# Kernel tuning notes

Hardware: AMD Instinct MI355X
Metric: run time of the kernel (lower is better)

## Reference

```python
import jax, jax.numpy as jnp
import numpy as np

DIM = 3072      # model dim (Qwen-Image)
HEADS = 24
HD = 128        # head dim; inner = HEADS*HD = 3072
INNER = HEADS * HD
FF = 4 * DIM    # 12288
S_IMG = 1024
S_TXT = 256
S_TOT = S_IMG + S_TXT
B = 1
EPS = 1e-6
SCALE_SHIFT = 1.0


def setup_inputs() -> dict:
    key = jax.random.key(0)
    ks = iter(jax.random.split(key, 64))
    W = 0.02

    def nrm(shape, s=W):
        return jax.random.normal(next(ks), shape, dtype=jnp.float32) * s

    # RoPE tables for the joint (txt first, then img) sequence, interleaved layout
    pos = jnp.arange(S_TOT, dtype=jnp.float32)
    inv = 1.0 / (10000.0 ** (jnp.arange(HD // 2, dtype=jnp.float32) / (HD // 2)))
    ang = pos[:, None] * inv[None, :]                       # [S, HD/2]
    rope_cos = jnp.repeat(jnp.cos(ang), 2, axis=-1)         # [S, HD]
    rope_sin = jnp.repeat(jnp.sin(ang), 2, axis=-1)

    inp = {
        "hidden_states": jax.random.normal(next(ks), (B, S_IMG, DIM), dtype=jnp.float32),
        "encoder_hidden_states": jax.random.normal(next(ks), (B, S_TXT, DIM), dtype=jnp.float32),
        "temb": jax.random.normal(next(ks), (B, DIM), dtype=jnp.float32),
        "rope_cos": rope_cos,
        "rope_sin": rope_sin,
        # modulation (AWQW4A16Linear equivalent)
        "img_mod_w": nrm((6 * DIM, DIM)), "img_mod_b": nrm((6 * DIM,)),
        "txt_mod_w": nrm((6 * DIM, DIM)), "txt_mod_b": nrm((6 * DIM,)),
        # attention (SVDQW4A4Linear equivalents)
        "qkv_w": nrm((3 * INNER, DIM)), "qkv_b": nrm((3 * INNER,)),
        "add_qkv_w": nrm((3 * INNER, DIM)), "add_qkv_b": nrm((3 * INNER,)),
        "norm_q_g": jnp.ones((HD,), jnp.float32), "norm_k_g": jnp.ones((HD,), jnp.float32),
        "norm_added_q_g": jnp.ones((HD,), jnp.float32), "norm_added_k_g": jnp.ones((HD,), jnp.float32),
        "to_out_w": nrm((DIM, INNER)), "to_out_b": nrm((DIM,)),
        "to_add_out_w": nrm((DIM, INNER)), "to_add_out_b": nrm((DIM,)),
        # MLPs
        "img_mlp_w1": nrm((FF, DIM)), "img_mlp_b1": nrm((FF,)),
        "img_mlp_w2": nrm((DIM, FF)), "img_mlp_b2": nrm((DIM,)),
        "txt_mlp_w1": nrm((FF, DIM)), "txt_mlp_b1": nrm((FF,)),
        "txt_mlp_w2": nrm((DIM, FF)), "txt_mlp_b2": nrm((DIM,)),
    }
    return inp


def _lin(x, w, b):
    return jnp.matmul(x, w.T) + b


def _ln(x):  # LayerNorm, no affine, eps=1e-6
    mu = jnp.mean(x, axis=-1, keepdims=True)
    var = jnp.mean(jnp.square(x - mu), axis=-1, keepdims=True)
    return (x - mu) * jax.lax.rsqrt(var + EPS)


def _rms(x, g):  # per-head RMSNorm over last dim (HD)
    ms = jnp.mean(jnp.square(x), axis=-1, keepdims=True)
    return x * jax.lax.rsqrt(ms + EPS) * g


def _rope(x, cos, sin):  # x: [B,S,H,D], cos/sin: [S,D], interleaved rotate
    x1 = x[..., 0::2]
    x2 = x[..., 1::2]
    xr = jnp.stack([-x2, x1], axis=-1).reshape(x.shape)
    return x * cos[None, :, None, :] + xr * sin[None, :, None, :]


def _reorder_mod(m):
    # view(B,-1,6).transpose(1,2).reshape(B,-1): de-interleave 6 modulation vecs
    b = m.shape[0]
    return m.reshape(b, DIM, 6).transpose(0, 2, 1).reshape(b, 6 * DIM)


def _modulate(x, mod):
    shift, scale, gate = jnp.split(mod, 3, axis=-1)
    return x * (scale + SCALE_SHIFT)[:, None, :] + shift[:, None, :], gate[:, None, :]


def _mlp(x, w1, b1, w2, b2):  # GELU(tanh) MLP
    h = jax.nn.gelu(_lin(x, w1, b1), approximate=True)
    return _lin(h, w2, b2)


def reference(hidden_states, encoder_hidden_states, temb, rope_cos, rope_sin,
              img_mod_w, img_mod_b, txt_mod_w, txt_mod_b,
              qkv_w, qkv_b, add_qkv_w, add_qkv_b,
              norm_q_g, norm_k_g, norm_added_q_g, norm_added_k_g,
              to_out_w, to_out_b, to_add_out_w, to_add_out_b,
              img_mlp_w1, img_mlp_b1, img_mlp_w2, img_mlp_b2,
              txt_mlp_w1, txt_mlp_b1, txt_mlp_w2, txt_mlp_b2):
    b = hidden_states.shape[0]

    img_mod = _reorder_mod(_lin(jax.nn.silu(temb), img_mod_w, img_mod_b))
    txt_mod = _reorder_mod(_lin(jax.nn.silu(temb), txt_mod_w, txt_mod_b))
    img_mod1, img_mod2 = jnp.split(img_mod, 2, axis=-1)
    txt_mod1, txt_mod2 = jnp.split(txt_mod, 2, axis=-1)

    img_modulated, img_gate1 = _modulate(_ln(hidden_states), img_mod1)
    txt_modulated, txt_gate1 = _modulate(_ln(encoder_hidden_states), txt_mod1)

    # ---- joint attention ----
    img_q, img_k, img_v = jnp.split(_lin(img_modulated, qkv_w, qkv_b), 3, axis=-1)
    txt_q, txt_k, txt_v = jnp.split(_lin(txt_modulated, add_qkv_w, add_qkv_b), 3, axis=-1)

    def heads(x):  # [B,S,INNER] -> [B,S,H,HD]
        return x.reshape(b, x.shape[1], HEADS, HD)

    img_q = _rms(heads(img_q), norm_q_g)
    img_k = _rms(heads(img_k), norm_k_g)
    txt_q = _rms(heads(txt_q), norm_added_q_g)
    txt_k = _rms(heads(txt_k), norm_added_k_g)

    q = jnp.concatenate([txt_q, img_q], axis=1)  # txt first
    k = jnp.concatenate([txt_k, img_k], axis=1)
    v = jnp.concatenate([heads(txt_v), heads(img_v)], axis=1)

    q = _rope(q, rope_cos, rope_sin)
    k = _rope(k, rope_cos, rope_sin)

    scale = 1.0 / jnp.sqrt(jnp.float32(HD))
    scores = jnp.einsum('bqhd,bkhd->bhqk', q, k) * scale
    probs = jax.nn.softmax(scores, axis=-1)
    attn = jnp.einsum('bhqk,bkhd->bqhd', probs, v).reshape(b, S_TOT, INNER)

    txt_attn = attn[:, :S_TXT, :]
    img_attn = attn[:, S_TXT:, :]
    img_attn = _lin(img_attn, to_out_w, to_out_b)
    txt_attn = _lin(txt_attn, to_add_out_w, to_add_out_b)

    hidden_states = hidden_states + img_gate1 * img_attn
    encoder_hidden_states = encoder_hidden_states + txt_gate1 * txt_attn

    # ---- MLPs ----
    img_m2, img_gate2 = _modulate(_ln(hidden_states), img_mod2)
    hidden_states = hidden_states + img_gate2 * _mlp(img_m2, img_mlp_w1, img_mlp_b1, img_mlp_w2, img_mlp_b2)

    txt_m2, txt_gate2 = _modulate(_ln(encoder_hidden_states), txt_mod2)
    encoder_hidden_states = encoder_hidden_states + txt_gate2 * _mlp(txt_m2, txt_mlp_w1, txt_mlp_b1, txt_mlp_w2, txt_mlp_b2)

    return (encoder_hidden_states, hidden_states)
```

## Files before the change

kernel.cpp:

```cpp
#include <hip/hip_runtime.h>

#define DIMC   3072
#define HEADS  24
#define HD     128
#define FF     12288
#define S_IMG  1024
#define S_TXT  256
#define S_TOT  1280
#define EPSF   1e-6f

typedef __attribute__((ext_vector_type(8))) short bf16x8;
typedef __attribute__((ext_vector_type(4))) float f32x4;
typedef __attribute__((ext_vector_type(4))) float float4v;
typedef __attribute__((ext_vector_type(4))) unsigned int u32x4;
typedef __attribute__((ext_vector_type(2))) unsigned int u32x2;

__device__ __forceinline__ unsigned short f2bf(float f) {
    union { float f; unsigned u; } c; c.f = f;
    unsigned u = c.u;
    unsigned r = (u + 0x7fffu + ((u >> 16) & 1u)) >> 16;
    return (unsigned short)r;
}
__device__ __forceinline__ float b2f(unsigned short h) {
    union { unsigned u; float f; } c; c.u = ((unsigned)h) << 16;
    return c.f;
}
__device__ __forceinline__ unsigned packbf(float a, float b) {
    union { float f; unsigned u; } x, y; x.f = a; y.f = b;
    return __builtin_amdgcn_perm(y.u + 0x8000u, x.u + 0x8000u, 0x07060302);
}
__device__ __forceinline__ float gelu_tanh(float v) {
    float u = 1.5957691216057308f * (v + 0.044715f * v * v * v);
    float e = __expf(u);
    float t = 1.0f - 2.0f / (e + 1.0f);
    return 0.5f * v * (1.0f + t);
}

#define GLL16(gsrc, ldst)                                                     \
    __builtin_amdgcn_global_load_lds(                                         \
        (const __attribute__((address_space(1))) void*)(gsrc),                \
        (__attribute__((address_space(3))) void*)(ldst), 16, 0, 0)

struct SwpArgs {
    const float* W;
    const unsigned short* X;
    const float* bias;
    unsigned short* out;
};

template<int EPI>
__global__ __launch_bounds__(512, 2)
void gemm_swp(SwpArgs g0, SwpArgs g1, int nxW, int padx, int K, int ldout)
{
    int bx, sTile;
    SwpArgs g;
    {
        const int id = blockIdx.x;
        const int imgN = padx * 4;
        if (id < imgN) {
            int xcd = id & 7, t = id >> 3;
            int j = t & 3, slot = t >> 2;
            bx = slot * 8 + xcd;
            if (bx >= nxW) return;
            g = g0; sTile = j * 256;
        } else {
            bx = id - imgN;
            g = g1; sTile = 0;
        }
    }
    const int bm = bx * 256;

    __shared__ __align__(16) char smem[131072];
    char* smemW = smem;
    char* smemX = smem + 65536;

    const int tid  = threadIdx.x;
    const int lane = tid & 63;
    const int wave = tid >> 6;
    const int wm = wave >> 2, wc = wave & 3;

    const int pW  = tid & 7;
    const int rW0 = tid >> 3;
    const int swW = (rW0 & 7) << 4;
    const int rX = lane >> 3;
    const int cX = (lane & 7) ^ rX;

    float4v wreg[4][2];

    auto WLOAD = [&](int t) {
        const float* src = g.W + (long)t * 64 + pW * 8;
        #pragma unroll
        for (int i = 0; i < 4; i++) {
            const float* p = src + (long)(bm + rW0 + i * 64) * K;
            wreg[i][0] = *(const float4v*)p;
            wreg[i][1] = *(const float4v*)(p + 4);
        }
    };
    auto WSTORE = [&](int buf) {
        #pragma unroll
        for (int i = 0; i < 4; i++) {
            int r = rW0 + i * 64;
            u32x4 w;
            w[0] = packbf(wreg[i][0][0], wreg[i][0][1]);
            w[1] = packbf(wreg[i][0][2], wreg[i][0][3]);
            w[2] = packbf(wreg[i][1][0], wreg[i][1][1]);
            w[3] = packbf(wreg[i][1][2], wreg[i][1][3]);
            *(u32x4*)(smemW + buf * 32768 + r * 128 + ((pW * 16) ^ swW)) = w;
        }
    };
    auto XSTAGE = [&](int buf, int t) {
        const long kof = (long)t * 64 + cX * 8;
        #pragma unroll
        for (int i = 0; i < 4; i++) {
            int r = i * 64 + wave * 8 + rX;
            GLL16(g.X + (long)(sTile + r) * K + kof,
                  smemX + buf * 32768 + i * 8192 + wave * 1024);
        }
    };

    f32x4 acc[8][4] = {};
    auto COMPUTE = [&](int buf) {
        #pragma unroll
        for (int ks = 0; ks < 2; ks++) {
            const int kb = ks * 64 + (lane >> 4) * 16;
            bf16x8 wf[8], xf[4];
            #pragma unroll
            for (int mi = 0; mi < 8; mi++) {
                int r = wm * 128 + mi * 16 + (lane & 15);
                wf[mi] = *(const bf16x8*)(smemW + buf * 32768 + r * 128 + (kb ^ ((r & 7) << 4)));
            }
            #pragma unroll
            for (int ni = 0; ni < 4; ni++) {
                int r = wc * 64 + ni * 16 + (lane & 15);
                xf[ni] = *(const bf16x8*)(smemX + buf * 32768 + r * 128 + (kb ^ ((r & 7) << 4)));
            }
            #pragma unroll
            for (int mi = 0; mi < 8; mi++)
                #pragma unroll
                for (int ni = 0; ni < 4; ni++)
                    acc[mi][ni] = __builtin_amdgcn_mfma_f32_16x16x32_bf16(
                        wf[mi], xf[ni], acc[mi][ni], 0, 0, 0);
        }
    };

    const int nk = K >> 6;
    WLOAD(0);
    XSTAGE(0, 0);
    WSTORE(0);
    __syncthreads();
    for (int t = 0; t < nk; ++t) {
        const int cur = t & 1;
        if (t + 1 < nk) {
            WLOAD(t + 1);
            XSTAGE(cur ^ 1, t + 1);
        }
        __builtin_amdgcn_sched_barrier(0);
        COMPUTE(cur);
        __builtin_amdgcn_sched_barrier(0);
        if (t + 1 < nk) WSTORE(cur ^ 1);
        __syncthreads();
    }

    #pragma unroll
    for (int mi = 0; mi < 8; mi++) {
        int m0 = wm * 128 + mi * 16 + ((lane >> 4) << 2);
        float4v bv = *(const float4v*)(g.bias + bm + m0);
        #pragma unroll
        for (int ni = 0; ni < 4; ni++) {
            int n = wc * 64 + ni * 16 + (lane & 15);
            float v0 = acc[mi][ni][0] + bv[0];
            float v1 = acc[mi][ni][1] + bv[1];
            float v2 = acc[mi][ni][2] + bv[2];
            float v3 = acc[mi][ni][3] + bv[3];
            if constexpr (EPI == 2) {
                v0 = gelu_tanh(v0); v1 = gelu_tanh(v1);
                v2 = gelu_tanh(v2); v3 = gelu_tanh(v3);
            }
            u32x2 w;
            w[0] = packbf(v0, v1);
            w[1] = packbf(v2, v3);
            *(u32x2*)(smem + n * 512 + ((2 * m0) ^ ((n & 31) << 4))) = w;
        }
    }
    __syncthreads();
    {
        const int s = tid >> 1;
        const int cbase = (tid & 1) * 16;
        unsigned short* orow = g.out + (long)(sTile + s) * ldout + bm;
        #pragma unroll
        for (int c = 0; c < 16; c++) {
            int chunk = cbase + c;
            u32x4 d = *(const u32x4*)(smem + s * 512 + ((chunk * 16) ^ ((s & 31) << 4)));
            *(u32x4*)(orow + chunk * 8) = d;
        }
    }
}

struct GemmArgs {
    const unsigned short* A;
    const void* B;
    const float* bias;
    void* out;
    long bOut;
};

template<int EPI, bool BF16B, bool SWZ>
__global__ __launch_bounds__(256)
void gemm_bt(GemmArgs g0, GemmArgs g1, int ysplit,
             int K, int lda, int ldb, int ldout,
             long batchA, long batchB, int nbn, int nby)
{
    int by, bnIdx, z;
    if constexpr (SWZ) {
        const int id = blockIdx.x;
        const int xcd = id & 7, t = id >> 3;
        const int j = t % 10;
        const int slot = t / 10;
        const int gidx = slot * 8 + xcd;
        by = j; bnIdx = gidx % nbn; z = gidx / nbn;
        (void)nby;
    } else {
        by = blockIdx.y; bnIdx = blockIdx.x; z = blockIdx.z;
    }

    __shared__ __align__(16) char smem[65536];
    char* smemA = smem;
    char* smemB = smem + 32768;

    const int tid  = threadIdx.x;
    const int lane = tid & 63;
    const int wave = tid >> 6;
    const int wm = wave >> 1, wc = wave & 1;

    const bool second = (by >= ysplit);
    const GemmArgs g = second ? g1 : g0;
    const int bm = (second ? by - ysplit : by) * 128;
    const int bn = bnIdx * 128;

    const unsigned short* A = g.A + (long)z * batchA;
    const float* Bf = (const float*)g.B + (long)z * batchB;
    const unsigned short* Bh = (const unsigned short*)g.B + (long)z * batchB;

    const int rA = lane >> 3;
    const int cA = (lane & 7) ^ rA;
    const int pB = tid & 7;
    const int rB0 = tid >> 3;
    const int swB = (rB0 & 7) << 4;

    float4v breg[4][2];

    auto BLOAD = [&](int t) {
        const float* src = Bf + (long)t * 64 + pB * 8;
        #pragma unroll
        for (int i = 0; i < 4; i++) {
            const float* p = src + (long)(bn + rB0 + i * 32) * ldb;
            breg[i][0] = *(const float4v*)p;
            breg[i][1] = *(const float4v*)(p + 4);
        }
    };
    auto STAGE_A = [&](int buf, int t) {
        const long kof = (long)t * 64 + cA * 8;
        #pragma unroll
        for (int i = 0; i < 4; i++) {
            int r = i * 32 + wave * 8 + rA;
            GLL16(A + (long)(bm + r) * lda + kof,
                  smemA + buf * 16384 + i * 4096 + wave * 1024);
        }
    };
    auto STAGE_B16 = [&](int buf, int t) {
        const long kof = (long)t * 64 + cA * 8;
        #pragma unroll
        for (int i = 0; i < 4; i++) {
            int r = i * 32 + wave * 8 + rA;
            GLL16(Bh + (long)(bn + r) * ldb + kof,
                  smemB + buf * 16384 + i * 4096 + wave * 1024);
        }
    };
    auto BSTORE = [&](int buf) {
        #pragma unroll
        for (int i = 0; i < 4; i++) {
            int r = rB0 + i * 32;
            u32x4 w;
            w[0] = packbf(breg[i][0][0], breg[i][0][1]);
            w[1] = packbf(breg[i][0][2], breg[i][0][3]);
            w[2] = packbf(breg[i][1][0], breg[i][1][1]);
            w[3] = packbf(breg[i][1][2], breg[i][1][3]);
            *(u32x4*)(smemB + buf * 16384 + r * 128 + ((pB * 16) ^ swB)) = w;
        }
    };

    f32x4 acc[4][4] = {};
    auto COMPUTE = [&](int buf) {
        #pragma unroll
        for (int ks = 0; ks < 2; ks++) {
            const int kb = ks * 64 + (lane >> 4) * 16;
            bf16x8 af[4], bfr[4];
            #pragma unroll
            for (int mi = 0; mi < 4; mi++) {
                int r = wm * 64 + mi * 16 + (lane & 15);
                af[mi] = *(const bf16x8*)(smemA + buf * 16384 + r * 128 + (kb ^ ((r & 7) << 4)));
            }
            #pragma unroll
            for (int ni = 0; ni < 4; ni++) {
                int r = wc * 64 + ni * 16 + (lane & 15);
                bfr[ni] = *(const bf16x8*)(smemB + buf * 16384 + r * 128 + (kb ^ ((r & 7) << 4)));
            }
            #pragma unroll
            for (int mi = 0; mi < 4; mi++)
                #pragma unroll
                for (int ni = 0; ni < 4; ni++)
                    acc[mi][ni] = __builtin_amdgcn_mfma_f32_16x16x32_bf16(
                        af[mi], bfr[ni], acc[mi][ni], 0, 0, 0);
        }
    };

    const int nk = K >> 6;
    if constexpr (BF16B) {
        STAGE_A(0, 0); STAGE_B16(0, 0);
    } else {
        BLOAD(0); STAGE_A(0, 0); BSTORE(0);
    }
    __syncthreads();
    for (int t = 0; t < nk; ++t) {
        const int cur = t & 1;
        if (t + 1 < nk) {
            if constexpr (BF16B) {
                STAGE_A(cur ^ 1, t + 1); STAGE_B16(cur ^ 1, t + 1);
            } else {
                BLOAD(t + 1); STAGE_A(cur ^ 1, t + 1);
            }
        }
        __builtin_amdgcn_sched_barrier(0);
        COMPUTE(cur);
        __builtin_amdgcn_sched_barrier(0);
        if constexpr (!BF16B) { if (t + 1 < nk) BSTORE(cur ^ 1); }
        __syncthreads();
    }

    unsigned short* outh = (unsigned short*)g.out + (long)z * g.bOut;
    float*          outf = (float*)g.out + (long)z * g.bOut;
    #pragma unroll
    for (int mi = 0; mi < 4; mi++) {
        #pragma unroll
        for (int ni = 0; ni < 4; ni++) {
            int n = bn + wc * 64 + ni * 16 + (lane & 15);
            float bv = g.bias ? g.bias[n] : 0.0f;
            #pragma unroll
            for (int r = 0; r < 4; r++) {
                int m = bm + wm * 64 + mi * 16 + (lane >> 4) * 4 + r;
                float v = acc[mi][ni][r] + bv;
                long o = (long)m * ldout + n;
                if constexpr (EPI == 0)      outf[o] = v;
                else                         outh[o] = f2bf(v);
            }
        }
    }
}

__global__ void silu_k(const float* __restrict__ x, float* __restrict__ out) {
    int i = blockIdx.x * 256 + threadIdx.x;
    if (i < DIMC) { float v = x[i]; out[i] = v / (1.0f + expf(-v)); }
}

__global__ __launch_bounds__(256)
void mod_gemv(const float* __restrict__ st,
              const float* __restrict__ Wimg, const float* __restrict__ bimg,
              const float* __restrict__ Wtxt, const float* __restrict__ btxt,
              float* __restrict__ mimg, float* __restrict__ mtxt)
{
    int wv = threadIdx.x >> 6, lane = threadIdx.x & 63;
    int r = blockIdx.x * 4 + wv;
    const float* W = blockIdx.y ? Wtxt : Wimg;
    const float* b = blockIdx.y ? btxt : bimg;
    float* out = blockIdx.y ? mtxt : mimg;
    const float* row = W + (long)r * DIMC;
    float acc = 0.f;
    #pragma unroll
    for (int j = 0; j < 12; j++) {
        float4v wvv = ((const float4v*)row)[lane + j * 64];
        float4v xv  = ((const float4v*)st)[lane + j * 64];
        acc += wvv[0] * xv[0] + wvv[1] * xv[1] + wvv[2] * xv[2] + wvv[3] * xv[3];
    }
    #pragma unroll
    for (int o = 32; o; o >>= 1) acc += __shfl_xor(acc, o);
    if (lane == 0) {
        int d = r / 6, j6 = r % 6;
        out[j6 * DIMC + d] = acc + b[r];
    }
}

__global__ __launch_bounds__(256)
void ln_mod(const float* __restrict__ x, const float* __restrict__ shift,
            const float* __restrict__ scale, unsigned short* __restrict__ out)
{
    __shared__ float red[8];
    long row = blockIdx.x;
    const float* xr = x + row * DIMC;
    float4v v[3];
    float sum = 0.f, sq = 0.f;
    #pragma unroll
    for (int j = 0; j < 3; j++) {
        v[j] = ((const float4v*)xr)[threadIdx.x + j * 256];
        #pragma unroll
        for (int c = 0; c < 4; c++) { sum += v[j][c]; sq += v[j][c] * v[j][c]; }
    }
    int lane = threadIdx.x & 63, wv = threadIdx.x >> 6;
    #pragma unroll
    for (int o = 32; o; o >>= 1) { sum += __shfl_xor(sum, o); sq += __shfl_xor(sq, o); }
    if (lane == 0) { red[wv] = sum; red[4 + wv] = sq; }
    __syncthreads();
    sum = red[0] + red[1] + red[2] + red[3];
    sq  = red[4] + red[5] + red[6] + red[7];
    float mu = sum / DIMC;
    float var = sq / DIMC - mu * mu;
    float rstd = rsqrtf(var + EPSF);
    #pragma unroll
    for (int j = 0; j < 3; j++) {
        int nb = (threadIdx.x + j * 256) * 4;
        #pragma unroll
        for (int c = 0; c < 4; c++) {
            int n = nb + c;
            float y = (v[j][c] - mu) * rstd * (scale[n] + 1.0f) + shift[n];
            out[row * DIMC + n] = f2bf(y);
        }
    }
}

__global__ __launch_bounds__(256)
void reduce_ln(const float* __restrict__ p0, const float* __restrict__ p1,
               const float* __restrict__ pbias, const float* __restrict__ base,
               const float* __restrict__ gate1, const float* __restrict__ shift2,
               const float* __restrict__ scale2,
               float* __restrict__ h1, unsigned short* __restrict__ mA)
{
    __shared__ float red[8];
    long off = (long)blockIdx.x * DIMC;
    float4v v[3];
    float sum = 0.f, sq = 0.f;
    #pragma unroll
    for (int j = 0; j < 3; j++) {
        int idx = threadIdx.x + j * 256;
        float4v a  = ((const float4v*)(base + off))[idx];
        float4v q0 = ((const float4v*)(p0 + off))[idx];
        float4v q1 = ((const float4v*)(p1 + off))[idx];
        float4v gb = ((const float4v*)pbias)[idx];
        float4v gt = ((const float4v*)gate1)[idx];
        #pragma unroll
        for (int c = 0; c < 4; c++) {
            float val = a[c] + gt[c] * (gb[c] + q0[c] + q1[c]);
            v[j][c] = val; sum += val; sq += val * val;
        }
        ((float4v*)(h1 + off))[idx] = v[j];
    }
    int lane = threadIdx.x & 63, wv = threadIdx.x >> 6;
    #pragma unroll
    for (int o = 32; o; o >>= 1) { sum += __shfl_xor(sum, o); sq += __shfl_xor(sq, o); }
    if (lane == 0) { red[wv] = sum; red[4 + wv] = sq; }
    __syncthreads();
    sum = red[0] + red[1] + red[2] + red[3];
    sq  = red[4] + red[5] + red[6] + red[7];
    float mu = sum / DIMC;
    float rstd = rsqrtf(sq / DIMC - mu * mu + EPSF);
    #pragma unroll
    for (int j = 0; j < 3; j++) {
        int nb = (threadIdx.x + j * 256) * 4;
        #pragma unroll
        for (int c = 0; c < 4; c++) {
            int n = nb + c;
            float y = (v[j][c] - mu) * rstd * (scale2[n] + 1.0f) + shift2[n];
            mA[off + n] = f2bf(y);
        }
    }
}

__global__ __launch_bounds__(256)
void reduce_out(const float* __restrict__ p, long PS,
                const float* __restrict__ h1, const float* __restrict__ wbias,
                const float* __restrict__ gate2, float* __restrict__ out, int n4)
{
    int i = blockIdx.x * 256 + threadIdx.x;
    if (i >= n4) return;
    int n = (i * 4) % DIMC;
    float4v s = ((const float4v*)p)[i];
    float4v s1 = ((const float4v*)(p + PS))[i];
    float4v s2 = ((const float4v*)(p + 2 * PS))[i];
    float4v s3 = ((const float4v*)(p + 3 * PS))[i];
    float4v h = ((const float4v*)h1)[i];
    float4v bv = *(const float4v*)(wbias + n);
    float4v gv = *(const float4v*)(gate2 + n);
    float4v r;
    #pragma unroll
    for (int c = 0; c < 4; c++)
        r[c] = h[c] + gv[c] * (bv[c] + s[c] + s1[c] + s2[c] + s3[c]);
    ((float4v*)out)[i] = r;
}

__global__ __launch_bounds__(256)
void qkv_post(const unsigned short* __restrict__ qkv_img,
              const unsigned short* __restrict__ qkv_txt,
              const float* __restrict__ nqg, const float* __restrict__ nkg,
              const float* __restrict__ naqg, const float* __restrict__ nakg,
              const float* __restrict__ rc, const float* __restrict__ rs,
              unsigned short* __restrict__ q, unsigned short* __restrict__ k,
              unsigned short* __restrict__ vt)
{
    int s = blockIdx.x;
    int h = blockIdx.y * 4 + (threadIdx.x >> 6);
    int d0 = threadIdx.x & 63;
    const unsigned short* src;
    const float *gq, *gk;
    if (s < S_TXT) { src = qkv_txt + (long)s * 3 * DIMC; gq = naqg; gk = nakg; }
    else           { src = qkv_img + (long)(s - S_TXT) * 3 * DIMC; gq = nqg; gk = nkg; }

    float q0 = b2f(src[h * HD + d0]),            q1 = b2f(src[h * HD + d0 + 64]);
    float k0 = b2f(src[DIMC + h * HD + d0]),     k1 = b2f(src[DIMC + h * HD + d0 + 64]);
    float v0 = b2f(src[2 * DIMC + h * HD + d0]), v1 = b2f(src[2 * DIMC + h * HD + d0 + 64]);

    float sqq = q0 * q0 + q1 * q1;
    float sqk = k0 * k0 + k1 * k1;
    #pragma unroll
    for (int o = 32; o; o >>= 1) { sqq += __shfl_xor(sqq, o); sqk += __shfl_xor(sqk, o); }
    float rq = rsqrtf(sqq / (float)HD + EPSF);
    float rk = rsqrtf(sqk / (float)HD + EPSF);
    q0 *= rq * gq[d0]; q1 *= rq * gq[d0 + 64];
    k0 *= rk * gk[d0]; k1 *= rk * gk[d0 + 64];

    float qp0 = __shfl_xor(q0, 1), qp1 = __shfl_xor(q1, 1);
    float kp0 = __shfl_xor(k0, 1), kp1 = __shfl_xor(k1, 1);
    float c0 = rc[(long)s * HD + d0], c1 = rc[(long)s * HD + d0 + 64];
    float s0 = rs[(long)s * HD + d0], s1 = rs[(long)s * HD + d0 + 64];
    float sgn = (d0 & 1) ? 1.0f : -1.0f;
    float qo0 = q0 * c0 + sgn * qp0 * s0;
    float qo1 = q1 * c1 + sgn * qp1 * s1;
    float ko0 = k0 * c0 + sgn * kp0 * s0;
    float ko1 = k1 * c1 + sgn * kp1 * s1;

    const float scl = 0.08838834764831845f;
    long qkbase = ((long)h * S_TOT + s) * HD;
    q[qkbase + d0]      = f2bf(qo0 * scl);
    q[qkbase + d0 + 64] = f2bf(qo1 * scl);
    k[qkbase + d0]      = f2bf(ko0);
    k[qkbase + d0 + 64] = f2bf(ko1);
    vt[((long)h * HD + d0) * S_TOT + s]        = f2bf(v0);
    vt[((long)h * HD + d0 + 64) * S_TOT + s]   = f2bf(v1);
}

__global__ __launch_bounds__(256)
void softmax_k(unsigned short* __restrict__ scores)
{
    long row = (long)blockIdx.x * 4 + (threadIdx.x >> 6);
    int lane = threadIdx.x & 63;
    unsigned short* p = scores + row * S_TOT;
    float v[20];
    float mx = -1e30f;
    #pragma unroll
    for (int j = 0; j < 20; j++) { v[j] = b2f(p[lane + j * 64]); mx = fmaxf(mx, v[j]); }
    #pragma unroll
    for (int o = 32; o; o >>= 1) mx = fmaxf(mx, __shfl_xor(mx, o));
    float sum = 0.f;
    #pragma unroll
    for (int j = 0; j < 20; j++) { v[j] = __expf(v[j] - mx); sum += v[j]; }
    #pragma unroll
    for (int o = 32; o; o >>= 1) sum += __shfl_xor(sum, o);
    float inv = 1.0f / sum;
    #pragma unroll
    for (int j = 0; j < 20; j++) p[lane + j * 64] = f2bf(v[j] * inv);
}

extern "C" void kernel_launch(void* const* d_in, const int* in_sizes, int n_in,
                              void* d_out, int out_size, void* d_ws, size_t ws_size,
                              hipStream_t stream)
{
    const float* hidden   = (const float*)d_in[0];
    const float* enc      = (const float*)d_in[1];
    const float* temb     = (const float*)d_in[2];
    const float* rope_cos = (const float*)d_in[3];
    const float* rope_sin = (const float*)d_in[4];
    const float* img_mod_w = (const float*)d_in[5];
    const float* img_mod_b = (const float*)d_in[6];
    const float* txt_mod_w = (const float*)d_in[7];
    const float* txt_mod_b = (const float*)d_in[8];
    const float* qkv_w     = (const float*)d_in[9];
    const float* qkv_b     = (const float*)d_in[10];
    const float* add_qkv_w = (const float*)d_in[11];
    const float* add_qkv_b = (const float*)d_in[12];
    const float* norm_q_g  = (const float*)d_in[13];
    const float* norm_k_g  = (const float*)d_in[14];
    const float* norm_aq_g = (const float*)d_in[15];
    const float* norm_ak_g = (const float*)d_in[16];
    const float* to_out_w  = (const float*)d_in[17];
    const float* to_out_b  = (const float*)d_in[18];
    const float* to_add_out_w = (const float*)d_in[19];
    const float* to_add_out_b = (const float*)d_in[20];
    const float* img_mlp_w1 = (const float*)d_in[21];
    const float* img_mlp_b1 = (const float*)d_in[22];
    const float* img_mlp_w2 = (const float*)d_in[23];
    const float* img_mlp_b2 = (const float*)d_in[24];
    const float* txt_mlp_w1 = (const float*)d_in[25];
    const float* txt_mlp_b1 = (const float*)d_in[26];
    const float* txt_mlp_w2 = (const float*)d_in[27];
    const float* txt_mlp_b2 = (const float*)d_in[28];

    char* w = (char*)d_ws;
    auto alloc = [&](size_t bytes) { char* p = w; w += (bytes + 255) & ~(size_t)255; return p; };
    float* silu_t  = (float*)alloc(DIMC * 4);
    float* mod_img = (float*)alloc(6 * DIMC * 4);
    float* mod_txt = (float*)alloc(6 * DIMC * 4);
    unsigned short* mA_img = (unsigned short*)alloc((long)S_IMG * DIMC * 2);
    unsigned short* mA_txt = (unsigned short*)alloc((long)S_TXT * DIMC * 2);
    unsigned short* qkv_img = (unsigned short*)alloc((long)S_IMG * 3 * DIMC * 2);
    unsigned short* qkv_txt = (unsigned short*)alloc((long)S_TXT * 3 * DIMC * 2);
    unsigned short* qb = (unsigned short*)alloc((long)HEADS * S_TOT * HD * 2);
    unsigned short* kb = (unsigned short*)alloc((long)HEADS * S_TOT * HD * 2);
    unsigned short* vt = (unsigned short*)alloc((long)HEADS * HD * S_TOT * 2);
    unsigned short* scores = (unsigned short*)alloc((long)HEADS * S_TOT * S_TOT * 2);
    unsigned short* attn = (unsigned short*)alloc((long)S_TOT * DIMC * 2);
    float* h1_img = (float*)alloc((long)S_IMG * DIMC * 4);
    float* h1_txt = (float*)alloc((long)S_TXT * DIMC * 4);
    unsigned short* gelu_img = (unsigned short*)alloc((long)S_IMG * FF * 2);
    unsigned short* gelu_txt = (unsigned short*)alloc((long)S_TXT * FF * 2);

    const long PS = (long)S_TOT * DIMC;
    float* part = (float*)scores;
    float* part_img = part;
    float* part_txt = part + (long)S_IMG * DIMC;

    float* out_enc = (float*)d_out;
    float* out_hid = (float*)d_out + (long)S_TXT * DIMC;

    silu_k<<<12, 256, 0, stream>>>(temb, silu_t);
    mod_gemv<<<dim3(4608, 2), 256, 0, stream>>>(silu_t, img_mod_w, img_mod_b,
                                                txt_mod_w, txt_mod_b, mod_img, mod_txt);

    ln_mod<<<S_IMG, 256, 0, stream>>>(hidden, mod_img, mod_img + DIMC, mA_img);
    ln_mod<<<S_TXT, 256, 0, stream>>>(enc, mod_txt, mod_txt + DIMC, mA_txt);

    {
        SwpArgs gi{qkv_w, mA_img, qkv_b, qkv_img};
        SwpArgs gt{add_qkv_w, mA_txt, add_qkv_b, qkv_txt};
        gemm_swp<1><<<40 * 4 + 36, 512, 0, stream>>>(gi, gt, 36, 40, DIMC, 3 * DIMC);
    }

    qkv_post<<<dim3(S_TOT, HEADS / 4), 256, 0, stream>>>(
        qkv_img, qkv_txt, norm_q_g, norm_k_g, norm_aq_g, norm_ak_g,
        rope_cos, rope_sin, qb, kb, vt);

    {
        GemmArgs gs{qb, kb, nullptr, scores, (long)S_TOT * S_TOT};
        gemm_bt<1, true, false><<<dim3(10, 10, HEADS), 256, 0, stream>>>(
            gs, gs, 10, HD, HD, HD, S_TOT,
            (long)S_TOT * HD, (long)S_TOT * HD, 0, 0);
    }
    softmax_k<<<(HEADS * S_TOT) / 4, 256, 0, stream>>>(scores);
    {
        GemmArgs gp{scores, vt, nullptr, attn, HD};
        gemm_bt<1, true, false><<<dim3(1, 10, HEADS), 256, 0, stream>>>(
            gp, gp, 10, S_TOT, S_TOT, S_TOT, DIMC,
            (long)S_TOT * S_TOT, (long)HD * S_TOT, 0, 0);
    }

    {
        GemmArgs gi{attn + (long)S_TXT * DIMC, to_out_w, nullptr, part_img, PS};
        GemmArgs gt{attn, to_add_out_w, nullptr, part_txt, PS};
        gemm_bt<0, false, true><<<24 * 2 * 10, 256, 0, stream>>>(
            gi, gt, 8, 1536, DIMC, DIMC, DIMC, 1536, 1536, 24, 10);
    }

    reduce_ln<<<S_IMG, 256, 0, stream>>>(
        part_img, part_img + PS, to_out_b, hidden,
        mod_img + 2 * DIMC, mod_img + 3 * DIMC, mod_img + 4 * DIMC,
        h1_img, mA_img);
    reduce_ln<<<S_TXT, 256, 0, stream>>>(
        part_txt, part_txt + PS, to_add_out_b, enc,
        mod_txt + 2 * DIMC, mod_txt + 3 * DIMC, mod_txt + 4 * DIMC,
        h1_txt, mA_txt);

    {
        SwpArgs gi{img_mlp_w1, mA_img, img_mlp_b1, gelu_img};
        SwpArgs gt{txt_mlp_w1, mA_txt, txt_mlp_b1, gelu_txt};
        gemm_swp<2><<<48 * 4 + 48, 512, 0, stream>>>(gi, gt, 48, 48, DIMC, FF);
    }

    {
        GemmArgs gi{gelu_img, img_mlp_w2, nullptr, part_img, PS};
        GemmArgs gt{gelu_txt, txt_mlp_w2, nullptr, part_txt, PS};
        gemm_bt<0, false, true><<<24 * 4 * 10, 256, 0, stream>>>(
            gi, gt, 8, 3072, FF, FF, DIMC, 3072, 3072, 24, 10);
    }
    reduce_out<<<(S_IMG * DIMC / 4 + 255) / 256, 256, 0, stream>>>(
        part_img, PS, h1_img, img_mlp_b2, mod_img + 5 * DIMC, out_hid,
        S_IMG * DIMC / 4);
    reduce_out<<<(S_TXT * DIMC / 4 + 255) / 256, 256, 0, stream>>>(
        part_txt, PS, h1_txt, txt_mlp_b2, mod_txt + 5 * DIMC, out_enc,
        S_TXT * DIMC / 4);
}
```

Baseline: 770.9 us.

## Split GEMM main loop into barrier-synchronized phases interleaving loads with MFMA

The GEMM K-loop is restructured into four phases, each reading half of the W fragments from LDS and running 16 MFMAs. Global prefetch of W, the X stage into LDS and the W store to LDS are spread across these phases. Each MFMA block is bracketed by s_barrier, explicit waitcnt and raised s_setprio so waves take turns between memory and matrix work. The aim is to overlap global and LDS traffic with tensor math and cut register pressure from holding all eight W fragments at once. The cost is extra barriers per iteration and stricter ordering that could stall waves.

```diff
diff --git a/kernel.cpp b/kernel.cpp
--- a/kernel.cpp
+++ b/kernel.cpp
@@ -119,47 +119,87 @@
     };
 
     f32x4 acc[8][4] = {};
-    auto COMPUTE = [&](int buf) {
-        #pragma unroll
-        for (int ks = 0; ks < 2; ks++) {
-            const int kb = ks * 64 + (lane >> 4) * 16;
-            bf16x8 wf[8], xf[4];
+
+    auto RD_W = [&](int buf, int ks, int mh, bf16x8* wf) {
+        const int kb = ks * 64 + (lane >> 4) * 16;
+        #pragma unroll
+        for (int j = 0; j < 4; j++) {
+            int r = wm * 128 + (mh * 4 + j) * 16 + (lane & 15);
+            wf[j] = *(const bf16x8*)(smemW + buf * 32768 + r * 128 + (kb ^ ((r & 7) << 4)));
+        }
+    };
+    auto RD_X = [&](int buf, int ks, bf16x8* xf) {
+        const int kb = ks * 64 + (lane >> 4) * 16;
+        #pragma unroll
+        for (int j = 0; j < 4; j++) {
+            int r = wc * 64 + j * 16 + (lane & 15);
+            xf[j] = *(const bf16x8*)(smemX + buf * 32768 + r * 128 + (kb ^ ((r & 7) << 4)));
+        }
+    };
+    auto MFMA16 = [&](int mh, const bf16x8* wf, const bf16x8* xf) {
+        #pragma unroll
+        for (int j = 0; j < 4; j++)
             #pragma unroll
-            for (int mi = 0; mi < 8; mi++) {
-                int r = wm * 128 + mi * 16 + (lane & 15);
-                wf[mi] = *(const bf16x8*)(smemW + buf * 32768 + r * 128 + (kb ^ ((r & 7) << 4)));
-            }
-            #pragma unroll
-            for (int ni = 0; ni < 4; ni++) {
-                int r = wc * 64 + ni * 16 + (lane & 15);
-                xf[ni] = *(const bf16x8*)(smemX + buf * 32768 + r * 128 + (kb ^ ((r & 7) << 4)));
-            }
-            #pragma unroll
-            for (int mi = 0; mi < 8; mi++)
-                #pragma unroll
-                for (int ni = 0; ni < 4; ni++)
-                    acc[mi][ni] = __builtin_amdgcn_mfma_f32_16x16x32_bf16(
-                        wf[mi], xf[ni], acc[mi][ni], 0, 0, 0);
-        }
-    };
+            for (int ni = 0; ni < 4; ni++)
+                acc[mh * 4 + j][ni] = __builtin_amdgcn_mfma_f32_16x16x32_bf16(
+                    wf[j], xf[ni], acc[mh * 4 + j][ni], 0, 0, 0);
+    };
+
+#define PHASE_SYNC_PRE                                                        \
+    __builtin_amdgcn_sched_barrier(0);                                        \
+    __builtin_amdgcn_s_barrier();                                             \
+    asm volatile("s_waitcnt lgkmcnt(0)" ::: "memory");                        \
+    __builtin_amdgcn_sched_barrier(0);                                        \
+    __builtin_amdgcn_s_setprio(1);
+#define PHASE_SYNC_POST                                                       \
+    __builtin_amdgcn_s_setprio(0);                                            \
+    __builtin_amdgcn_sched_barrier(0);                                        \
+    __builtin_amdgcn_s_barrier();
 
     const int nk = K >> 6;
     WLOAD(0);
     XSTAGE(0, 0);
     WSTORE(0);
-    __syncthreads();
+    asm volatile("s_waitcnt vmcnt(0) lgkmcnt(0)" ::: "memory");
+    __builtin_amdgcn_sched_barrier(0);
+    __builtin_amdgcn_s_barrier();
+
     for (int t = 0; t < nk; ++t) {
         const int cur = t & 1;
-        if (t + 1 < nk) {
-            WLOAD(t + 1);
-            XSTAGE(cur ^ 1, t + 1);
-        }
+        const bool pf = (t + 1 < nk);
+        bf16x8 wf[4], xf[4];
+
+        RD_X(cur, 0, xf);
+        RD_W(cur, 0, 0, wf);
+        if (pf) WLOAD(t + 1);
+        PHASE_SYNC_PRE
+        MFMA16(0, wf, xf);
+        PHASE_SYNC_POST
+
+        RD_W(cur, 0, 1, wf);
+        if (pf) XSTAGE(cur ^ 1, t + 1);
+        PHASE_SYNC_PRE
+        MFMA16(1, wf, xf);
+        PHASE_SYNC_POST
+
+        RD_X(cur, 1, xf);
+        RD_W(cur, 1, 0, wf);
+        PHASE_SYNC_PRE
+        MFMA16(0, wf, xf);
+        PHASE_SYNC_POST
+
+        RD_W(cur, 1, 1, wf);
+        if (pf) WSTORE(cur ^ 1);
+        PHASE_SYNC_PRE
+        MFMA16(1, wf, xf);
+        __builtin_amdgcn_s_setprio(0);
         __builtin_amdgcn_sched_barrier(0);
-        COMPUTE(cur);
+        asm volatile("s_waitcnt vmcnt(0)" ::: "memory");
         __builtin_amdgcn_sched_barrier(0);
-        if (t + 1 < nk) WSTORE(cur ^ 1);
-        __syncthreads();
-    }
+        __builtin_amdgcn_s_barrier();
+    }
+#undef PHASE_SYNC_PRE
+#undef PHASE_SYNC_POST
 
     #pragma unroll
     for (int mi = 0; mi < 8; mi++) {
```

After: 768.8 us. No clear change (-0.3%).
